# Optimization experiments

Hardware: AMD Instinct MI355X
Metric: run time of the kernel (lower is better)

Reference implementation:

```python
import jax, jax.numpy as jnp
import numpy as np

EPS = 1e-8  # matches torch F.cosine_similarity default eps


def setup_inputs() -> dict:
    key = jax.random.key(0)
    k0, k1, k2, k3 = jax.random.split(key, 4)
    B, S, H, D, E = 8, 128, 768, 256, 50000
    return {
        "hidden_states": jax.random.normal(k0, (B, S, H), dtype=jnp.float32),
        "W": jax.random.normal(k1, (D, H), dtype=jnp.float32) * 0.02,
        "b": jnp.zeros((D,), dtype=jnp.float32),
        "md_W": jax.random.normal(k2, (3, H), dtype=jnp.float32) * 0.02,
        "md_b": jnp.zeros((3,), dtype=jnp.float32),
        "entity_embedding": jax.random.normal(k3, (E, D), dtype=jnp.float32),
    }


def reference(hidden_states, W, b, md_W, md_b, entity_embedding):
    # Mention detection head: linear + log_softmax over dim=1 (seq dim, as in torch code)
    md_logits = jnp.einsum("bsh,ch->bsc", hidden_states, md_W) + md_b  # [B,S,3]
    md_out = jax.nn.log_softmax(md_logits, axis=1)

    # Entity disambiguation head: linear -> tanh -> cosine similarity vs entity table.
    # cosine_similarity(a,b) = <a,b> / (max(||a||,eps) * max(||b||,eps)); expressed as
    # L2-normalize both sides then a single GEMM (mathematically identical, no [B,S,E,D] broadcast).
    proj = jnp.tanh(jnp.einsum("bsh,dh->bsd", hidden_states, W) + b)  # [B,S,D]
    proj_n = proj / jnp.maximum(jnp.linalg.norm(proj, axis=-1, keepdims=True), EPS)
    ent_n = entity_embedding / jnp.maximum(
        jnp.linalg.norm(entity_embedding, axis=-1, keepdims=True), EPS
    )
    similarity = jnp.einsum("bsd,ed->bse", proj_n, ent_n)  # [B,S,E]
    return (md_out, similarity)
```

## Files before the change

### kernel.cpp

```cpp
#include <hip/hip_runtime.h>
#include <cstdint>
#include <cstddef>

#define Bz 8
#define Sz 128
#define Hz 768
#define Dz 256
#define Ez 50000
#define Mz (Bz*Sz)
#define EPAD 50048

#define ENT_BLOCKS  12512
#define CONV_BLOCKS 960
#define MD_BLOCKS   256
#define FRONT_BLOCKS (ENT_BLOCKS + CONV_BLOCKS + MD_BLOCKS)

typedef __bf16 bf16x8 __attribute__((ext_vector_type(8)));
typedef float  f32x4  __attribute__((ext_vector_type(4)));

__device__ __forceinline__ unsigned short f2bf(float f) {
  unsigned int u = __float_as_uint(f);
  u += 0x7fffu + ((u >> 16) & 1u);
  return (unsigned short)(u >> 16);
}

#define GLOAD_LDS16(gp, lp) \
  __builtin_amdgcn_global_load_lds((__attribute__((address_space(1))) void*)(gp), \
                                   (__attribute__((address_space(3))) void*)(lp), 16, 0, 0)

__global__ __launch_bounds__(256) void k_front(
    const float* __restrict__ hid, const float* __restrict__ W,
    const float* __restrict__ mdW, const float* __restrict__ mdb,
    const float* __restrict__ ent,
    ushort4* __restrict__ hb, ushort4* __restrict__ wb,
    ushort4* __restrict__ en, float* __restrict__ lt) {
  const int tid  = threadIdx.x;
  const int lane = tid & 63;
  const int wave = tid >> 6;
  int blk = blockIdx.x;

  if (blk < ENT_BLOCKS) {
    int row = blk * 4 + wave;
    if (row >= Ez) {
      en[(size_t)row*64 + lane] = make_ushort4(0,0,0,0);
      return;
    }
    float4 v = ((const float4*)ent)[(size_t)row*64 + lane];
    float ss = v.x*v.x + v.y*v.y + v.z*v.z + v.w*v.w;
    #pragma unroll
    for (int off = 32; off > 0; off >>= 1) ss += __shfl_xor(ss, off, 64);
    float inv = 1.f / fmaxf(sqrtf(ss), 1e-8f);
    ushort4 o;
    o.x = f2bf(v.x*inv); o.y = f2bf(v.y*inv); o.z = f2bf(v.z*inv); o.w = f2bf(v.w*inv);
    en[(size_t)row*64 + lane] = o;
    return;
  }
  blk -= ENT_BLOCKS;

  if (blk < CONV_BLOCKS) {
    int i = blk * 256 + tid;
    float4 v = (i < 196608) ? ((const float4*)hid)[i] : ((const float4*)W)[i - 196608];
    ushort4 o;
    o.x = f2bf(v.x); o.y = f2bf(v.y); o.z = f2bf(v.z); o.w = f2bf(v.w);
    if (i < 196608) hb[i] = o; else wb[i - 196608] = o;
    return;
  }
  blk -= CONV_BLOCKS;

  int row = blk * 4 + wave;
  const float4* hr = (const float4*)hid + (size_t)row*192 + lane*3;
  float4 a0 = hr[0], a1 = hr[1], a2 = hr[2];
  const float4* w4 = (const float4*)mdW;
  float p[3];
  #pragma unroll
  for (int c = 0; c < 3; ++c) {
    float4 w0 = w4[c*192 + lane*3], w1 = w4[c*192 + lane*3 + 1], w2 = w4[c*192 + lane*3 + 2];
    p[c] = a0.x*w0.x + a0.y*w0.y + a0.z*w0.z + a0.w*w0.w
         + a1.x*w1.x + a1.y*w1.y + a1.z*w1.z + a1.w*w1.w
         + a2.x*w2.x + a2.y*w2.y + a2.z*w2.z + a2.w*w2.w;
  }
  #pragma unroll
  for (int c = 0; c < 3; ++c)
    #pragma unroll
    for (int off = 32; off > 0; off >>= 1) p[c] += __shfl_xor(p[c], off, 64);
  if (lane == 0) {
    #pragma unroll
    for (int c = 0; c < 3; ++c) lt[c*Mz + row] = p[c] + mdb[c];
  }
}

__global__ void k_md_softmax(const float* __restrict__ lt, float* __restrict__ out) {
  int b = blockIdx.x / 3, c = blockIdx.x % 3;
  int s = threadIdx.x;
  float logit = lt[c*Mz + b*Sz + s];
  __shared__ float red[Sz];
  red[s] = logit; __syncthreads();
  for (int off = 64; off > 0; off >>= 1) {
    if (s < off) red[s] = fmaxf(red[s], red[s+off]);
    __syncthreads();
  }
  float mx = red[0]; __syncthreads();
  red[s] = expf(logit - mx); __syncthreads();
  for (int off = 64; off > 0; off >>= 1) {
    if (s < off) red[s] += red[s+off];
    __syncthreads();
  }
  float lse = mx + logf(red[0]);
  out[(size_t)(b*Sz + s)*3 + c] = logit - lse;
}

__global__ __launch_bounds__(256, 1) void k_proj_norm(
    const unsigned short* __restrict__ A,
    const unsigned short* __restrict__ Bm,
    const float* __restrict__ bias,
    unsigned short* __restrict__ Pn) {
  __shared__ unsigned short Alds[128*32];
  __shared__ unsigned short Blds[256*32];
  __shared__ float ssq2[128][2];
  const int tid  = threadIdx.x;
  const int lane = tid & 63;
  const int wave = tid >> 6;
  const int m0 = blockIdx.x * 128;
  const int wm = (wave >> 1) * 64;
  const int wn = (wave & 1) * 128;
  const int srow   = lane >> 2;
  const int schunk = lane & 3;
  const unsigned short* Agb = A  + (size_t)(m0 + wave*32 + srow)*Hz + schunk*8;
  const unsigned short* Bgb = Bm + (size_t)(wave*64 + srow)*Hz + schunk*8;
  unsigned short* AL0 = &Alds[(wave*32)*32];
  unsigned short* AL1 = &Alds[(wave*32+16)*32];

  f32x4 acc[4][8];
  f32x4 z = {0.f,0.f,0.f,0.f};
  #pragma unroll
  for (int i = 0; i < 4; ++i)
    #pragma unroll
    for (int j = 0; j < 8; ++j) acc[i][j] = z;

  const int kof = (lane >> 4) * 8;
  const int fr  = lane & 15;

  for (int kt = 0; kt < Hz; kt += 32) {
    GLOAD_LDS16(Agb + kt,                 AL0);
    GLOAD_LDS16(Agb + 16*(size_t)Hz + kt, AL1);
    #pragma unroll
    for (int c = 0; c < 4; ++c)
      GLOAD_LDS16(Bgb + c*16*(size_t)Hz + kt, &Blds[(wave*64 + c*16)*32]);
    __syncthreads();
    bf16x8 af[4], bq[8];
    #pragma unroll
    for (int mi = 0; mi < 4; ++mi)
      af[mi] = *(const bf16x8*)&Alds[(wm + mi*16 + fr)*32 + kof];
    #pragma unroll
    for (int ni = 0; ni < 8; ++ni)
      bq[ni] = *(const bf16x8*)&Blds[(wn + ni*16 + fr)*32 + kof];
    #pragma unroll
    for (int mi = 0; mi < 4; ++mi)
      #pragma unroll
      for (int ni = 0; ni < 8; ++ni)
        acc[mi][ni] = __builtin_amdgcn_mfma_f32_16x16x32_bf16(af[mi], bq[ni], acc[mi][ni], 0, 0, 0);
    __syncthreads();
  }

  const int rl = wm + (lane >> 4) * 4;
  #pragma unroll
  for (int mi = 0; mi < 4; ++mi) {
    #pragma unroll
    for (int reg = 0; reg < 4; ++reg) {
      float s = 0.f;
      #pragma unroll
      for (int ni = 0; ni < 8; ++ni) {
        float v = tanhf(acc[mi][ni][reg] + bias[wn + ni*16 + fr]);
        acc[mi][ni][reg] = v;
        s += v*v;
      }
      s += __shfl_xor(s, 1, 64); s += __shfl_xor(s, 2, 64);
      s += __shfl_xor(s, 4, 64); s += __shfl_xor(s, 8, 64);
      if ((lane & 15) == 0) ssq2[rl + mi*16 + reg][wave & 1] = s;
    }
  }
  __syncthreads();
  #pragma unroll
  for (int mi = 0; mi < 4; ++mi) {
    #pragma unroll
    for (int reg = 0; reg < 4; ++reg) {
      int r = rl + mi*16 + reg;
      float inv = 1.f / fmaxf(sqrtf(ssq2[r][0] + ssq2[r][1]), 1e-8f);
      #pragma unroll
      for (int ni = 0; ni < 8; ++ni)
        Pn[(size_t)(m0 + r)*Dz + wn + ni*16 + fr] = f2bf(acc[mi][ni][reg] * inv);
    }
  }
}

__global__ __launch_bounds__(256) void k_sim(
    const unsigned short* __restrict__ A, const unsigned short* __restrict__ Bm,
    float* __restrict__ C) {
  __shared__ unsigned short Alds[128*32];
  __shared__ unsigned short Blds[128*32];
  const int tid  = threadIdx.x;
  const int lane = tid & 63;
  const int wave = tid >> 6;
  const int m0 = blockIdx.x * 128;
  const int n0 = blockIdx.y * 128;
  const int wm = (wave >> 1) * 64;
  const int wn = (wave & 1) * 64;
  const int srow   = lane >> 2;
  const int schunk = lane & 3;
  const unsigned short* Agb = A  + (size_t)(m0 + wave*32 + srow)*Dz + schunk*8;
  const unsigned short* Bgb = Bm + (size_t)(n0 + wave*32 + srow)*Dz + schunk*8;
  unsigned short* Al0 = &Alds[(wave*32)*32];
  unsigned short* Al1 = &Alds[(wave*32+16)*32];
  unsigned short* Bl0 = &Blds[(wave*32)*32];
  unsigned short* Bl1 = &Blds[(wave*32+16)*32];

  f32x4 acc[4][4];
  f32x4 z = {0.f,0.f,0.f,0.f};
  #pragma unroll
  for (int i = 0; i < 4; ++i)
    #pragma unroll
    for (int j = 0; j < 4; ++j) acc[i][j] = z;

  const int kof = (lane >> 4) * 8;
  const int fr  = lane & 15;

  for (int kt = 0; kt < Dz; kt += 32) {
    GLOAD_LDS16(Agb + kt,                 Al0);
    GLOAD_LDS16(Agb + 16*(size_t)Dz + kt, Al1);
    GLOAD_LDS16(Bgb + kt,                 Bl0);
    GLOAD_LDS16(Bgb + 16*(size_t)Dz + kt, Bl1);
    __syncthreads();
    bf16x8 af[4], bq[4];
    #pragma unroll
    for (int mi = 0; mi < 4; ++mi)
      af[mi] = *(const bf16x8*)&Alds[(wm + mi*16 + fr)*32 + kof];
    #pragma unroll
    for (int ni = 0; ni < 4; ++ni)
      bq[ni] = *(const bf16x8*)&Blds[(wn + ni*16 + fr)*32 + kof];
    #pragma unroll
    for (int mi = 0; mi < 4; ++mi)
      #pragma unroll
      for (int ni = 0; ni < 4; ++ni)
        acc[mi][ni] = __builtin_amdgcn_mfma_f32_16x16x32_bf16(af[mi], bq[ni], acc[mi][ni], 0, 0, 0);
    __syncthreads();
  }

  const int rbase = m0 + wm + (lane >> 4) * 4;
  const int cbase = n0 + wn + (lane & 15);
  #pragma unroll
  for (int mi = 0; mi < 4; ++mi) {
    #pragma unroll
    for (int ni = 0; ni < 4; ++ni) {
      int n = cbase + ni*16;
      if (n < Ez) {
        #pragma unroll
        for (int reg = 0; reg < 4; ++reg) {
          int m = rbase + mi*16 + reg;
          C[(size_t)m * Ez + n] = acc[mi][ni][reg];
        }
      }
    }
  }
}

extern "C" void kernel_launch(void* const* d_in, const int* in_sizes, int n_in,
                              void* d_out, int out_size, void* d_ws, size_t ws_size,
                              hipStream_t stream) {
  (void)in_sizes; (void)n_in; (void)out_size; (void)ws_size;
  const float* hid = (const float*)d_in[0];
  const float* W   = (const float*)d_in[1];
  const float* bb  = (const float*)d_in[2];
  const float* mdW = (const float*)d_in[3];
  const float* mdb = (const float*)d_in[4];
  const float* ent = (const float*)d_in[5];
  float* out = (float*)d_out;

  char* ws = (char*)d_ws;
  unsigned short* hb = (unsigned short*)(ws);
  unsigned short* wb = (unsigned short*)(ws + 1572864);
  unsigned short* pn = (unsigned short*)(ws + 1966080);
  float*          lt = (float*)         (ws + 2490368);
  unsigned short* en = (unsigned short*)(ws + 2502656);

  k_front<<<FRONT_BLOCKS, 256, 0, stream>>>(hid, W, mdW, mdb, ent,
                                            (ushort4*)hb, (ushort4*)wb, (ushort4*)en, lt);
  k_md_softmax<<<Bz*3, Sz, 0, stream>>>(lt, out);
  k_proj_norm<<<8, 256, 0, stream>>>(hb, wb, bb, pn);
  k_sim<<<dim3(8, 391), 256, 0, stream>>>(pn, en, out + (size_t)Mz*3);
}
```

Baseline: 349.0 us.

## Split projection GEMM over more blocks, swizzle sim grid, use nontemporal stores

```diff
diff --git a/kernel.cpp b/kernel.cpp
--- a/kernel.cpp
+++ b/kernel.cpp
@@ -114,81 +114,79 @@
     const unsigned short* __restrict__ Bm,
     const float* __restrict__ bias,
     unsigned short* __restrict__ Pn) {
-  __shared__ unsigned short Alds[128*32];
+  __shared__ unsigned short Alds[32*32];
   __shared__ unsigned short Blds[256*32];
-  __shared__ float ssq2[128][2];
+  __shared__ float ssq[32][4];
   const int tid  = threadIdx.x;
   const int lane = tid & 63;
   const int wave = tid >> 6;
-  const int m0 = blockIdx.x * 128;
-  const int wm = (wave >> 1) * 64;
-  const int wn = (wave & 1) * 128;
+  const int m0 = blockIdx.x * 32;
   const int srow   = lane >> 2;
   const int schunk = lane & 3;
-  const unsigned short* Agb = A  + (size_t)(m0 + wave*32 + srow)*Hz + schunk*8;
+  const unsigned short* Agb = A  + (size_t)(m0 + srow)*Hz + schunk*8;
   const unsigned short* Bgb = Bm + (size_t)(wave*64 + srow)*Hz + schunk*8;
-  unsigned short* AL0 = &Alds[(wave*32)*32];
-  unsigned short* AL1 = &Alds[(wave*32+16)*32];
-
-  f32x4 acc[4][8];
+
+  f32x4 acc[2][4];
   f32x4 z = {0.f,0.f,0.f,0.f};
   #pragma unroll
-  for (int i = 0; i < 4; ++i)
-    #pragma unroll
-    for (int j = 0; j < 8; ++j) acc[i][j] = z;
+  for (int i = 0; i < 2; ++i)
+    #pragma unroll
+    for (int j = 0; j < 4; ++j) acc[i][j] = z;
 
   const int kof = (lane >> 4) * 8;
   const int fr  = lane & 15;
 
   for (int kt = 0; kt < Hz; kt += 32) {
-    GLOAD_LDS16(Agb + kt,                 AL0);
-    GLOAD_LDS16(Agb + 16*(size_t)Hz + kt, AL1);
+    if (wave == 0) {
+      GLOAD_LDS16(Agb + kt,                 &Alds[0]);
+      GLOAD_LDS16(Agb + 16*(size_t)Hz + kt, &Alds[16*32]);
+    }
     #pragma unroll
     for (int c = 0; c < 4; ++c)
       GLOAD_LDS16(Bgb + c*16*(size_t)Hz + kt, &Blds[(wave*64 + c*16)*32]);
     __syncthreads();
-    bf16x8 af[4], bq[8];
-    #pragma unroll
-    for (int mi = 0; mi < 4; ++mi)
-      af[mi] = *(const bf16x8*)&Alds[(wm + mi*16 + fr)*32 + kof];
-    #pragma unroll
-    for (int ni = 0; ni < 8; ++ni)
-      bq[ni] = *(const bf16x8*)&Blds[(wn + ni*16 + fr)*32 + kof];
-    #pragma unroll
-    for (int mi = 0; mi < 4; ++mi)
-      #pragma unroll
-      for (int ni = 0; ni < 8; ++ni)
+    bf16x8 af[2], bq[4];
+    #pragma unroll
+    for (int mi = 0; mi < 2; ++mi)
+      af[mi] = *(const bf16x8*)&Alds[(mi*16 + fr)*32 + kof];
+    #pragma unroll
+    for (int ni = 0; ni < 4; ++ni)
+      bq[ni] = *(const bf16x8*)&Blds[(wave*64 + ni*16 + fr)*32 + kof];
+    #pragma unroll
+    for (int mi = 0; mi < 2; ++mi)
+      #pragma unroll
+      for (int ni = 0; ni < 4; ++ni)
         acc[mi][ni] = __builtin_amdgcn_mfma_f32_16x16x32_bf16(af[mi], bq[ni], acc[mi][ni], 0, 0, 0);
     __syncthreads();
   }
 
-  const int rl = wm + (lane >> 4) * 4;
-  #pragma unroll
-  for (int mi = 0; mi < 4; ++mi) {
+  const int rl = (lane >> 4) * 4;
+  #pragma unroll
+  for (int mi = 0; mi < 2; ++mi) {
     #pragma unroll
     for (int reg = 0; reg < 4; ++reg) {
       float s = 0.f;
       #pragma unroll
-      for (int ni = 0; ni < 8; ++ni) {
-        float v = tanhf(acc[mi][ni][reg] + bias[wn + ni*16 + fr]);
+      for (int ni = 0; ni < 4; ++ni) {
+        float v = tanhf(acc[mi][ni][reg] + bias[wave*64 + ni*16 + fr]);
         acc[mi][ni][reg] = v;
         s += v*v;
       }
       s += __shfl_xor(s, 1, 64); s += __shfl_xor(s, 2, 64);
       s += __shfl_xor(s, 4, 64); s += __shfl_xor(s, 8, 64);
-      if ((lane & 15) == 0) ssq2[rl + mi*16 + reg][wave & 1] = s;
+      if ((lane & 15) == 0) ssq[mi*16 + rl + reg][wave] = s;
     }
   }
   __syncthreads();
   #pragma unroll
-  for (int mi = 0; mi < 4; ++mi) {
+  for (int mi = 0; mi < 2; ++mi) {
     #pragma unroll
     for (int reg = 0; reg < 4; ++reg) {
-      int r = rl + mi*16 + reg;
-      float inv = 1.f / fmaxf(sqrtf(ssq2[r][0] + ssq2[r][1]), 1e-8f);
-      #pragma unroll
-      for (int ni = 0; ni < 8; ++ni)
-        Pn[(size_t)(m0 + r)*Dz + wn + ni*16 + fr] = f2bf(acc[mi][ni][reg] * inv);
+      int r = mi*16 + rl + reg;
+      float inv = 1.f / fmaxf(sqrtf(ssq[r][0] + ssq[r][1] + ssq[r][2] + ssq[r][3]), 1e-8f);
+      #pragma unroll
+      for (int ni = 0; ni < 4; ++ni)
+        Pn[(size_t)(m0 + r)*Dz + wave*64 + ni*16 + fr] = f2bf(acc[mi][ni][reg] * inv);
     }
   }
 }
@@ -201,8 +199,9 @@
   const int tid  = threadIdx.x;
   const int lane = tid & 63;
   const int wave = tid >> 6;
-  const int m0 = blockIdx.x * 128;
-  const int n0 = blockIdx.y * 128;
+  const int w  = (blockIdx.x & 7) * 391 + (blockIdx.x >> 3);
+  const int m0 = (w & 7) * 128;
+  const int n0 = (w >> 3) * 128;
   const int wm = (wave >> 1) * 64;
   const int wn = (wave & 1) * 64;
   const int srow   = lane >> 2;
@@ -256,7 +255,7 @@
         #pragma unroll
         for (int reg = 0; reg < 4; ++reg) {
           int m = rbase + mi*16 + reg;
-          C[(size_t)m * Ez + n] = acc[mi][ni][reg];
+          __builtin_nontemporal_store(acc[mi][ni][reg], &C[(size_t)m * Ez + n]);
         }
       }
     }
@@ -285,6 +284,6 @@
   k_front<<<FRONT_BLOCKS, 256, 0, stream>>>(hid, W, mdW, mdb, ent,
                                             (ushort4*)hb, (ushort4*)wb, (ushort4*)en, lt);
   k_md_softmax<<<Bz*3, Sz, 0, stream>>>(lt, out);
-  k_proj_norm<<<8, 256, 0, stream>>>(hb, wb, bb, pn);
-  k_sim<<<dim3(8, 391), 256, 0, stream>>>(pn, en, out + (size_t)Mz*3);
-}
+  k_proj_norm<<<32, 256, 0, stream>>>(hb, wb, bb, pn);
+  k_sim<<<3128, 256, 0, stream>>>(pn, en, out + (size_t)Mz*3);
+}
```

Result: faster. 313.1 us (median of 2 runs) (-10.3%).
